# Kernel optimization log

Hardware: AMD Instinct MI355X
Metric: run time of the kernel (lower is better)

## Reference

```python
import jax, jax.numpy as jnp
import numpy as np

NX, NY = 8192, 8192
FX, FY = 1024, 1024
EMB, EMB_OUT = 512, 512


def setup_inputs() -> dict:
    key = jax.random.key(0)
    ks = jax.random.split(key, 8)
    s = lambda f: 1.0 / np.sqrt(f)
    return {
        "x": jax.random.normal(ks[0], (NX, FX), jnp.float32),
        "y": jax.random.normal(ks[1], (NY, FY), jnp.float32),
        "Wx": jax.random.uniform(ks[2], (FX, EMB), jnp.float32, -s(FX), s(FX)),
        "bx": jax.random.uniform(ks[3], (EMB,), jnp.float32, -s(FX), s(FX)),
        "Wy": jax.random.uniform(ks[4], (FY, EMB), jnp.float32, -s(FY), s(FY)),
        "by": jax.random.uniform(ks[5], (EMB,), jnp.float32, -s(FY), s(FY)),
        "Wg": jax.random.uniform(ks[6], (EMB, EMB_OUT), jnp.float32, -s(EMB), s(EMB)),
        "bg": jax.random.uniform(ks[7], (EMB_OUT,), jnp.float32, -s(EMB), s(EMB)),
    }


def reference(x, y, Wx, bx, Wy, by, Wg, bg):
    # Linear projections: [Nx, emb], [Ny, emb]
    xp = x @ Wx + bx
    yp = y @ Wy + by
    # Pairwise affinity (Dice-coefficient style normalization)
    A_ = xp @ yp.T                              # [Nx, Ny]
    Dcol = jnp.sum(xp * xp, axis=1)[:, None]    # ||x_i||^2, diag of xp@xp.T
    Drow = jnp.sum(yp * yp, axis=1)[None, :]    # ||y_j||^2, diag of yp@yp.T
    A = 2.0 * A_ / (Dcol + Drow)                # [Nx, Ny]
    # Weighted aggregation over x nodes, then ReLU MLP
    gwf = A.T @ xp                              # [Ny, emb]
    return jax.nn.relu(gwf @ Wg + bg)           # [Ny, emb_out]
```

## Files before the change

### kernel.cpp

```cpp
#include <hip/hip_runtime.h>
#include <hip/hip_bf16.h>


typedef __attribute__((ext_vector_type(8))) short bf16x8;
typedef __attribute__((ext_vector_type(4))) short bf16x4;
typedef __attribute__((ext_vector_type(4))) float f32x4;

__device__ __forceinline__ short f2b(float f) {
    unsigned int u = __builtin_bit_cast(unsigned int, f);
    unsigned int r = (u + 0x7fffu + ((u >> 16) & 1u)) >> 16;
    return (short)r;
}
__device__ __forceinline__ float b2f(short s) {
    unsigned int u = ((unsigned int)(unsigned short)s) << 16;
    return __builtin_bit_cast(float, u);
}

__device__ __forceinline__ void cp16(const void* g, void* l) {
    __builtin_amdgcn_global_load_lds(
        (const __attribute__((address_space(1))) void*)g,
        (__attribute__((address_space(3))) void*)l, 16, 0, 0);
}

constexpr int EPI_XP = 0;
constexpr int EPI_BF = 1;
constexpr int EPI_AT = 2;

constexpr int ASRC_BF16 = 0;
constexpr int ASRC_F32  = 1;

template<int EPI, int ASRC, int TM, int TN>
__device__ __forceinline__ void gemm_core(
    const void* __restrict__ Aptr, int lda,
    const short* __restrict__ Bt, int ldb,
    int N, int K, int bm, int bn, int kbase,
    const float* __restrict__ bias,
    short* __restrict__ outb,
    float* __restrict__ Dacc,
    const float* __restrict__ Drow, const float* __restrict__ Dcol)
{
    constexpr int WN  = (TN >= 128) ? 2 : 1;
    constexpr int WM  = 4 / WN;
    constexpr int FRN = TN / WN / 16;
    constexpr int FRM = TM / WM / 16;
    __shared__ __align__(16) short As[TM * 32];
    __shared__ __align__(16) short Bs[TN * 32];

    const int tid  = threadIdx.x;
    const int wave = tid >> 6;
    const int lane = tid & 63;
    const int quad = lane >> 4;
    const int l15  = lane & 15;
    const int wn   = (wave % WN) * (FRN * 16);
    const int wm   = (wave / WN) * (FRM * 16);

    f32x4 acc[FRM][FRN];
#pragma unroll
    for (int i = 0; i < FRM; i++)
#pragma unroll
        for (int j = 0; j < FRN; j++) acc[i][j] = f32x4{0.f, 0.f, 0.f, 0.f};

    for (int k0 = kbase; k0 < kbase + K; k0 += 32) {
        if (ASRC == ASRC_F32) {
            const float* Af = (const float*)Aptr;
#pragma unroll
            for (int s = 0; s < TM * 8 / 256; s++) {
                const int seg = tid + 256 * s;
                const int row = seg >> 3, c4 = seg & 7;
                const float4 v = *(const float4*)&Af[(size_t)(bm + row) * lda + k0 + c4 * 4];
                bf16x4 b;
                b[0] = f2b(v.x); b[1] = f2b(v.y); b[2] = f2b(v.z); b[3] = f2b(v.w);
                *(bf16x4*)&As[row * 32 + c4 * 4] = b;
            }
        } else {
            const short* Ab = (const short*)Aptr;
#pragma unroll
            for (int s = 0; s < TM / 64; s++) {
                const int seg = tid + 256 * s;
                const int row = seg >> 2, c8 = seg & 3;
                cp16(&Ab[(size_t)(bm + row) * lda + k0 + c8 * 8], &As[seg * 8]);
            }
        }
#pragma unroll
        for (int s = 0; s < TN / 64; s++) {
            const int seg = tid + 256 * s;
            const int row = seg >> 2, c8 = seg & 3;
            cp16(&Bt[(size_t)(bn + row) * ldb + k0 + c8 * 8], &Bs[seg * 8]);
        }
        __syncthreads();

        bf16x8 a[FRM], b[FRN];
#pragma unroll
        for (int i = 0; i < FRM; i++)
            a[i] = *(const bf16x8*)&As[(wm + i * 16 + l15) * 32 + quad * 8];
#pragma unroll
        for (int j = 0; j < FRN; j++)
            b[j] = *(const bf16x8*)&Bs[(wn + j * 16 + l15) * 32 + quad * 8];
#pragma unroll
        for (int i = 0; i < FRM; i++)
#pragma unroll
            for (int j = 0; j < FRN; j++)
                acc[i][j] = __builtin_amdgcn_mfma_f32_16x16x32_bf16(a[i], b[j], acc[i][j], 0, 0, 0);
        __syncthreads();
    }

#pragma unroll
    for (int im = 0; im < FRM; ++im) {
#pragma unroll
        for (int r = 0; r < 4; ++r) {
            const int gm = bm + wm + im * 16 + quad * 4 + r;
            if (EPI == EPI_XP) {
                float s = 0.f;
#pragma unroll
                for (int jn = 0; jn < FRN; ++jn) {
                    const int gn = bn + wn + jn * 16 + l15;
                    const float v = acc[im][jn][r] + bias[gn];
                    outb[(size_t)gm * N + gn] = f2b(v);
                    s += v * v;
                }
#pragma unroll
                for (int m = 1; m < 16; m <<= 1) s += __shfl_xor(s, m, 64);
                if (l15 == 0) atomicAdd(&Dacc[gm], s);
            } else if (EPI == EPI_BF) {
#pragma unroll
                for (int jn = 0; jn < FRN; ++jn) {
                    const int gn = bn + wn + jn * 16 + l15;
                    outb[(size_t)gm * N + gn] = f2b(acc[im][jn][r]);
                }
            } else {
                const float dy = Drow[gm];
#pragma unroll
                for (int jn = 0; jn < FRN; ++jn) {
                    const int gn = bn + wn + jn * 16 + l15;
                    const float v = 2.f * acc[im][jn][r] * __builtin_amdgcn_rcpf(Dcol[gn] + dy);
                    outb[(size_t)gm * N + gn] = f2b(v);
                }
            }
        }
    }
}

__global__ __launch_bounds__(256)
void k_proj(const float* __restrict__ A, const short* __restrict__ Bt,
            const float* __restrict__ bias, short* __restrict__ outb,
            float* __restrict__ Dacc)
{
    gemm_core<EPI_XP, ASRC_F32, 64, 128>(A, 1024, Bt, 1024, 512, 1024,
                                         blockIdx.y * 64, blockIdx.x * 128, 0,
                                         bias, outb, Dacc, nullptr, nullptr);
}

__global__ __launch_bounds__(256)
void k_zT(const short* __restrict__ WgT, const short* __restrict__ xpb,
          short* __restrict__ zT)
{
    gemm_core<EPI_BF, ASRC_BF16, 64, 128>(WgT, 512, xpb, 512, 8192, 512,
                                          blockIdx.y * 64, blockIdx.x * 128, 0,
                                          nullptr, zT, nullptr, nullptr, nullptr);
}

__global__ __launch_bounds__(256, 2)
void k_aff(const short* __restrict__ ypb, const short* __restrict__ xpb,
           short* __restrict__ At, const float* __restrict__ Dy,
           const float* __restrict__ Dx)
{
    const int flat = blockIdx.x;
    const int xcd = flat & 7;
    const int q   = flat >> 3;
    const int st  = q >> 5;
    const int w   = q & 31;
    const int s   = xcd * 8 + st;
    const int bx  = (s & 7) * 4 + (w & 3);
    const int by  = (s >> 3) * 8 + (w >> 2);
    gemm_core<EPI_AT, ASRC_BF16, 128, 256>(ypb, 512, xpb, 512, 8192, 512,
                                           by * 128, bx * 256, 0,
                                           nullptr, At, nullptr, Dy, Dx);
}

__global__ __launch_bounds__(256)
void k_agg(const short* __restrict__ At, const short* __restrict__ zT,
           short* __restrict__ p0, short* __restrict__ p1)
{
    const int flat = blockIdx.x;
    const int xcd = flat & 7;
    const int q   = flat >> 3;
    const int g   = xcd * 16 + (q >> 3);
    const int bm  = (g >> 1) * 128;
    const int z   = g & 1;
    const int bn  = (q & 7) * 64;
    short* outb = z ? p1 : p0;
    gemm_core<EPI_BF, ASRC_BF16, 128, 64>(At, 8192, zT, 8192, 512, 4096,
                                          bm, bn, z * 4096,
                                          nullptr, outb, nullptr, nullptr, nullptr);
}

__global__ __launch_bounds__(256)
void k_fin(const short* __restrict__ p0, const short* __restrict__ p1,
           const float* __restrict__ bg, float* __restrict__ out)
{
    const int idx = (blockIdx.x * 256 + threadIdx.x) * 8;
    const int col = idx & 511;
    const bf16x8 a = *(const bf16x8*)&p0[idx];
    const bf16x8 b = *(const bf16x8*)&p1[idx];
    const f32x4 g0 = *(const f32x4*)&bg[col];
    const f32x4 g1 = *(const f32x4*)&bg[col + 4];
    f32x4 o0, o1;
#pragma unroll
    for (int e = 0; e < 4; ++e) {
        o0[e] = fmaxf(b2f(a[e]) + b2f(b[e]) + g0[e], 0.f);
        o1[e] = fmaxf(b2f(a[e + 4]) + b2f(b[e + 4]) + g1[e], 0.f);
    }
    *(f32x4*)&out[idx]     = o0;
    *(f32x4*)&out[idx + 4] = o1;
}

__global__ __launch_bounds__(256)
void transpose_f32_bf16(const float* __restrict__ in, short* __restrict__ out, int R, int C)
{
    __shared__ short t[32][33];
    const int tx = threadIdx.x, ty = threadIdx.y;
    const int bx = blockIdx.x * 32, by = blockIdx.y * 32;
#pragma unroll
    for (int i = 0; i < 32; i += 8)
        t[ty + i][tx] = f2b(in[(size_t)(by + ty + i) * C + bx + tx]);
    __syncthreads();
#pragma unroll
    for (int i = 0; i < 32; i += 8)
        out[(size_t)(bx + ty + i) * R + by + tx] = t[tx][ty + i];
}

extern "C" void kernel_launch(void* const* d_in, const int* in_sizes, int n_in,
                              void* d_out, int out_size, void* d_ws, size_t ws_size,
                              hipStream_t stream)
{
    const float* x  = (const float*)d_in[0];
    const float* y  = (const float*)d_in[1];
    const float* Wx = (const float*)d_in[2];
    const float* bx = (const float*)d_in[3];
    const float* Wy = (const float*)d_in[4];
    const float* by = (const float*)d_in[5];
    const float* Wg = (const float*)d_in[6];
    const float* bg = (const float*)d_in[7];
    float* out = (float*)d_out;

    char* p = (char*)d_ws;
    short* At   = (short*)p; p += (size_t)8192 * 8192 * 2;
    short* xpb  = (short*)p; p += (size_t)8192 * 512 * 2;
    short* ypb  = (short*)p; p += (size_t)8192 * 512 * 2;
    short* zT   = (short*)p; p += (size_t)512 * 8192 * 2;
    short* WxT  = (short*)p; p += (size_t)512 * 1024 * 2;
    short* WyT  = (short*)p; p += (size_t)512 * 1024 * 2;
    short* WgT  = (short*)p; p += (size_t)512 * 512 * 2;
    float* Dx   = (float*)p; p += (size_t)8192 * 4;
    float* Dy   = (float*)p; p += (size_t)8192 * 4;
    short* p0 = xpb;
    short* p1 = ypb;

    hipMemsetAsync(Dx, 0, 2 * 8192 * sizeof(float), stream);

    dim3 tb(32, 8);
    transpose_f32_bf16<<<dim3(512 / 32, 1024 / 32), tb, 0, stream>>>(Wx, WxT, 1024, 512);
    transpose_f32_bf16<<<dim3(512 / 32, 1024 / 32), tb, 0, stream>>>(Wy, WyT, 1024, 512);
    transpose_f32_bf16<<<dim3(512 / 32, 512 / 32),  tb, 0, stream>>>(Wg, WgT, 512, 512);

    k_proj<<<dim3(4, 128), 256, 0, stream>>>(x, WxT, bx, xpb, Dx);
    k_proj<<<dim3(4, 128), 256, 0, stream>>>(y, WyT, by, ypb, Dy);

    k_zT<<<dim3(64, 8), 256, 0, stream>>>(WgT, xpb, zT);

    k_aff<<<2048, 256, 0, stream>>>(ypb, xpb, At, Dy, Dx);

    k_agg<<<1024, 256, 0, stream>>>(At, zT, p0, p1);

    k_fin<<<2048, 256, 0, stream>>>(p0, p1, bg, out);
}
```

Before: 389.1 us.

## Swizzle LDS tiles with XOR layout and pre-convert inputs to bf16

```diff
diff --git a/kernel.cpp b/kernel.cpp
--- a/kernel.cpp
+++ b/kernel.cpp
@@ -26,12 +26,9 @@
 constexpr int EPI_BF = 1;
 constexpr int EPI_AT = 2;
 
-constexpr int ASRC_BF16 = 0;
-constexpr int ASRC_F32  = 1;
-
-template<int EPI, int ASRC, int TM, int TN>
+template<int EPI, int TM, int TN>
 __device__ __forceinline__ void gemm_core(
-    const void* __restrict__ Aptr, int lda,
+    const short* __restrict__ A, int lda,
     const short* __restrict__ Bt, int ldb,
     int N, int K, int bm, int bn, int kbase,
     const float* __restrict__ bias,
@@ -61,41 +58,33 @@
         for (int j = 0; j < FRN; j++) acc[i][j] = f32x4{0.f, 0.f, 0.f, 0.f};
 
     for (int k0 = kbase; k0 < kbase + K; k0 += 32) {
-        if (ASRC == ASRC_F32) {
-            const float* Af = (const float*)Aptr;
-#pragma unroll
-            for (int s = 0; s < TM * 8 / 256; s++) {
-                const int seg = tid + 256 * s;
-                const int row = seg >> 3, c4 = seg & 7;
-                const float4 v = *(const float4*)&Af[(size_t)(bm + row) * lda + k0 + c4 * 4];
-                bf16x4 b;
-                b[0] = f2b(v.x); b[1] = f2b(v.y); b[2] = f2b(v.z); b[3] = f2b(v.w);
-                *(bf16x4*)&As[row * 32 + c4 * 4] = b;
-            }
-        } else {
-            const short* Ab = (const short*)Aptr;
-#pragma unroll
-            for (int s = 0; s < TM / 64; s++) {
-                const int seg = tid + 256 * s;
-                const int row = seg >> 2, c8 = seg & 3;
-                cp16(&Ab[(size_t)(bm + row) * lda + k0 + c8 * 8], &As[seg * 8]);
-            }
+#pragma unroll
+        for (int s = 0; s < TM / 64; s++) {
+            const int seg = tid + 256 * s;
+            const int row = seg >> 2, c8 = seg & 3;
+            const int gg  = c8 ^ (row & 3);
+            cp16(&A[(size_t)(bm + row) * lda + k0 + gg * 8], &As[seg * 8]);
         }
 #pragma unroll
         for (int s = 0; s < TN / 64; s++) {
             const int seg = tid + 256 * s;
             const int row = seg >> 2, c8 = seg & 3;
-            cp16(&Bt[(size_t)(bn + row) * ldb + k0 + c8 * 8], &Bs[seg * 8]);
+            const int gg  = c8 ^ (row & 3);
+            cp16(&Bt[(size_t)(bn + row) * ldb + k0 + gg * 8], &Bs[seg * 8]);
         }
         __syncthreads();
 
         bf16x8 a[FRM], b[FRN];
 #pragma unroll
-        for (int i = 0; i < FRM; i++)
-            a[i] = *(const bf16x8*)&As[(wm + i * 16 + l15) * 32 + quad * 8];
-#pragma unroll
-        for (int j = 0; j < FRN; j++)
-            b[j] = *(const bf16x8*)&Bs[(wn + j * 16 + l15) * 32 + quad * 8];
+        for (int i = 0; i < FRM; i++) {
+            const int row = wm + i * 16 + l15;
+            a[i] = *(const bf16x8*)&As[row * 32 + ((quad ^ (row & 3)) << 3)];
+        }
+#pragma unroll
+        for (int j = 0; j < FRN; j++) {
+            const int row = wn + j * 16 + l15;
+            b[j] = *(const bf16x8*)&Bs[row * 32 + ((quad ^ (row & 3)) << 3)];
+        }
 #pragma unroll
         for (int i = 0; i < FRM; i++)
 #pragma unroll
@@ -141,22 +130,22 @@
 }
 
 __global__ __launch_bounds__(256)
-void k_proj(const float* __restrict__ A, const short* __restrict__ Bt,
+void k_proj(const short* __restrict__ A, const short* __restrict__ Bt,
             const float* __restrict__ bias, short* __restrict__ outb,
             float* __restrict__ Dacc)
 {
-    gemm_core<EPI_XP, ASRC_F32, 64, 128>(A, 1024, Bt, 1024, 512, 1024,
-                                         blockIdx.y * 64, blockIdx.x * 128, 0,
-                                         bias, outb, Dacc, nullptr, nullptr);
+    gemm_core<EPI_XP, 64, 128>(A, 1024, Bt, 1024, 512, 1024,
+                               blockIdx.y * 64, blockIdx.x * 128, 0,
+                               bias, outb, Dacc, nullptr, nullptr);
 }
 
 __global__ __launch_bounds__(256)
 void k_zT(const short* __restrict__ WgT, const short* __restrict__ xpb,
           short* __restrict__ zT)
 {
-    gemm_core<EPI_BF, ASRC_BF16, 64, 128>(WgT, 512, xpb, 512, 8192, 512,
-                                          blockIdx.y * 64, blockIdx.x * 128, 0,
-                                          nullptr, zT, nullptr, nullptr, nullptr);
+    gemm_core<EPI_BF, 64, 128>(WgT, 512, xpb, 512, 8192, 512,
+                               blockIdx.y * 64, blockIdx.x * 128, 0,
+                               nullptr, zT, nullptr, nullptr, nullptr);
 }
 
 __global__ __launch_bounds__(256, 2)
@@ -172,9 +161,9 @@
     const int s   = xcd * 8 + st;
     const int bx  = (s & 7) * 4 + (w & 3);
     const int by  = (s >> 3) * 8 + (w >> 2);
-    gemm_core<EPI_AT, ASRC_BF16, 128, 256>(ypb, 512, xpb, 512, 8192, 512,
-                                           by * 128, bx * 256, 0,
-                                           nullptr, At, nullptr, Dy, Dx);
+    gemm_core<EPI_AT, 128, 256>(ypb, 512, xpb, 512, 8192, 512,
+                                by * 128, bx * 256, 0,
+                                nullptr, At, nullptr, Dy, Dx);
 }
 
 __global__ __launch_bounds__(256)
@@ -189,9 +178,9 @@
     const int z   = g & 1;
     const int bn  = (q & 7) * 64;
     short* outb = z ? p1 : p0;
-    gemm_core<EPI_BF, ASRC_BF16, 128, 64>(At, 8192, zT, 8192, 512, 4096,
-                                          bm, bn, z * 4096,
-                                          nullptr, outb, nullptr, nullptr, nullptr);
+    gemm_core<EPI_BF, 128, 64>(At, 8192, zT, 8192, 512, 4096,
+                               bm, bn, z * 4096,
+                               nullptr, outb, nullptr, nullptr, nullptr);
 }
 
 __global__ __launch_bounds__(256)
@@ -212,6 +201,16 @@
     }
     *(f32x4*)&out[idx]     = o0;
     *(f32x4*)&out[idx + 4] = o1;
+}
+
+__global__ __launch_bounds__(256)
+void k_cvt(const float* __restrict__ in, short* __restrict__ out)
+{
+    const int i = (blockIdx.x * 256 + threadIdx.x) * 4;
+    const float4 v = *(const float4*)&in[i];
+    bf16x4 b;
+    b[0] = f2b(v.x); b[1] = f2b(v.y); b[2] = f2b(v.z); b[3] = f2b(v.w);
+    *(bf16x4*)&out[i] = b;
 }
 
 __global__ __launch_bounds__(256)
@@ -244,7 +243,10 @@
     float* out = (float*)d_out;
 
     char* p = (char*)d_ws;
-    short* At   = (short*)p; p += (size_t)8192 * 8192 * 2;
+    short* At   = (short*)p;
+    short* xb   = (short*)p;
+    short* yb   = (short*)(p + (size_t)8192 * 1024 * 2);
+    p += (size_t)8192 * 8192 * 2;
     short* xpb  = (short*)p; p += (size_t)8192 * 512 * 2;
     short* ypb  = (short*)p; p += (size_t)8192 * 512 * 2;
     short* zT   = (short*)p; p += (size_t)512 * 8192 * 2;
@@ -263,8 +265,11 @@
     transpose_f32_bf16<<<dim3(512 / 32, 1024 / 32), tb, 0, stream>>>(Wy, WyT, 1024, 512);
     transpose_f32_bf16<<<dim3(512 / 32, 512 / 32),  tb, 0, stream>>>(Wg, WgT, 512, 512);
 
-    k_proj<<<dim3(4, 128), 256, 0, stream>>>(x, WxT, bx, xpb, Dx);
-    k_proj<<<dim3(4, 128), 256, 0, stream>>>(y, WyT, by, ypb, Dy);
+    k_cvt<<<8192, 256, 0, stream>>>(x, xb);
+    k_cvt<<<8192, 256, 0, stream>>>(y, yb);
+
+    k_proj<<<dim3(4, 128), 256, 0, stream>>>(xb, WxT, bx, xpb, Dx);
+    k_proj<<<dim3(4, 128), 256, 0, stream>>>(yb, WyT, by, ypb, Dy);
 
     k_zT<<<dim3(64, 8), 256, 0, stream>>>(WgT, xpb, zT);
 
```

New measurement: 372.2 us. -4.3%, faster.
